# Kernel tuning notes

Measured on AMD Instinct MI355X. Metric: run time of the kernel, lower is better.

Reference implementation:

```python
import jax, jax.numpy as jnp
import numpy as np

B = 32; NPG = 290; N = B * NPG; EPG = 2320; E = B * EPG
LP = 900; IN_FEATS = 75; D = 128; HD = 256; K = 3; HK = HD * K; HOUT = 2


def setup_inputs() -> dict:
    key = jax.random.key(0)
    ks = jax.random.split(key, 20)
    s = 0.05
    rng = np.random.default_rng(0)
    off = np.arange(B)[:, None] * NPG  # keep edges inside each graph block
    edge_src = jnp.asarray((rng.integers(0, NPG, (B, EPG)) + off).reshape(-1), dtype=jnp.int32)
    edge_dst = jnp.asarray((rng.integers(0, NPG, (B, EPG)) + off).reshape(-1), dtype=jnp.int32)
    node_h = jax.random.normal(ks[0], (N, IN_FEATS), jnp.float32)
    v_p = jax.random.randint(ks[1], (B, LP), 0, 26, jnp.int32)
    W_init = (jax.random.normal(ks[2], (IN_FEATS, D)) * s).at[:, -1].set(0.0)  # padding unit zeroed
    gcn_W = jax.random.normal(ks[3], (3, 3, D, D)) * s
    gcn_b = jnp.zeros((3, 3, D))
    gcn_Wres = jax.random.normal(ks[4], (3, 3, D, D)) * s
    gcn_bres = jnp.zeros((3, 3, D))
    emb = (jax.random.normal(ks[5], (26, D)) * s).at[0].set(0.0)  # padding_idx=0
    conv1_w = jax.random.normal(ks[6], (D, D, 3)) * s
    conv2_w = jax.random.normal(ks[7], (D, D, 6)) * s
    conv3_w = jax.random.normal(ks[8], (D, D, 9)) * s
    conv_b = jnp.zeros((3, D))
    cnn_bn_g = jnp.ones((3, D)); cnn_bn_b = jnp.zeros((3, D))
    Wv = jax.random.normal(ks[9], (D, HK)) * s; bv = jnp.zeros((HK,))
    Wq = jax.random.normal(ks[10], (D, HK)) * s; bq = jnp.zeros((HK,))
    h_mat = jax.random.normal(ks[11], (HOUT, HK)) * s
    h_bias = jnp.zeros((HOUT,))
    ban_bn_g = jnp.ones((HD,)); ban_bn_b = jnp.zeros((HD,))
    m_w1 = jax.random.normal(ks[12], (HD, 512)) * s; m_b1 = jnp.zeros((512,))
    m_w2 = jax.random.normal(ks[13], (512, 512)) * s; m_b2 = jnp.zeros((512,))
    m_w3 = jax.random.normal(ks[14], (512, 128)) * s; m_b3 = jnp.zeros((128,))
    m_w4 = jax.random.normal(ks[15], (128, 1)) * s; m_b4 = jnp.zeros((1,))
    mbn_g1 = jnp.ones((512,)); mbn_b1 = jnp.zeros((512,))
    mbn_g2 = jnp.ones((512,)); mbn_b2 = jnp.zeros((512,))
    mbn_g3 = jnp.ones((128,)); mbn_b3 = jnp.zeros((128,))
    return dict(node_h=node_h, edge_src=edge_src, edge_dst=edge_dst, v_p=v_p,
                W_init=W_init, gcn_W=gcn_W, gcn_b=gcn_b, gcn_Wres=gcn_Wres, gcn_bres=gcn_bres,
                emb=emb, conv1_w=conv1_w, conv2_w=conv2_w, conv3_w=conv3_w, conv_b=conv_b,
                cnn_bn_g=cnn_bn_g, cnn_bn_b=cnn_bn_b, Wv=Wv, bv=bv, Wq=Wq, bq=bq,
                h_mat=h_mat, h_bias=h_bias, ban_bn_g=ban_bn_g, ban_bn_b=ban_bn_b,
                m_w1=m_w1, m_b1=m_b1, m_w2=m_w2, m_b2=m_b2, m_w3=m_w3, m_b3=m_b3,
                m_w4=m_w4, m_b4=m_b4, mbn_g1=mbn_g1, mbn_b1=mbn_b1, mbn_g2=mbn_g2,
                mbn_b2=mbn_b2, mbn_g3=mbn_g3, mbn_b3=mbn_b3)


def _bn_feat(x, g, b):  # BatchNorm1d on [B, C], training-mode batch stats
    m = jnp.mean(x, 0); v = jnp.var(x, 0)
    return (x - m) * jax.lax.rsqrt(v + 1e-5) * g + b


def _bn_chan(x, g, b):  # BatchNorm1d on [B, C, L]
    m = jnp.mean(x, (0, 2), keepdims=True); v = jnp.var(x, (0, 2), keepdims=True)
    return (x - m) * jax.lax.rsqrt(v + 1e-5) * g[None, :, None] + b[None, :, None]


def _forward(node_h, W_init, gcn_W, gcn_b, gcn_Wres, gcn_bres, emb, conv1_w, conv2_w,
             conv3_w, conv_b, cnn_bn_g, cnn_bn_b, Wv, bv, Wq, bq, h_mat, h_bias,
             ban_bn_g, ban_bn_b, m_w1, m_b1, m_w2, m_b2, m_w3, m_b3, m_w4, m_b4,
             mbn_g1, mbn_b1, mbn_g2, mbn_b2, mbn_g3, mbn_b3, edge_src, edge_dst, v_p):
    relu = jax.nn.relu

    def gcn(h, W, b, Wr, br):  # 3 dgllife GCN layers: sum-aggregate + relu + residual
        for l in range(3):
            agg = jax.ops.segment_sum(h[edge_src], edge_dst, num_segments=N)
            h = relu(agg @ W[l] + b[l]) + relu(h @ Wr[l] + br[l])
        return h

    h0 = node_h @ W_init  # shared init_transform (no bias)
    v_d_o = gcn(h0, gcn_W[0], gcn_b[0], gcn_Wres[0], gcn_bres[0]).reshape(B, NPG, D)
    pos1 = gcn(h0, gcn_W[1], gcn_b[1], gcn_Wres[1], gcn_bres[1]).reshape(B, NPG, D)
    pos2 = gcn(h0, gcn_W[2], gcn_b[2], gcn_Wres[2], gcn_bres[2]).reshape(B, NPG, D)

    x = emb[v_p].transpose(0, 2, 1)  # [B, D, LP]
    dn = ('NCH', 'OIH', 'NCH')
    for w, cb, g, bb in ((conv1_w, conv_b[0], cnn_bn_g[0], cnn_bn_b[0]),
                         (conv2_w, conv_b[1], cnn_bn_g[1], cnn_bn_b[1]),
                         (conv3_w, conv_b[2], cnn_bn_g[2], cnn_bn_b[2])):
        x = jax.lax.conv_general_dilated(x, w, (1,), 'VALID', dimension_numbers=dn) + cb[None, :, None]
        x = _bn_chan(relu(x), g, bb)
    v_p_o = x.transpose(0, 2, 1)  # [B, 885, D]

    q_ = relu(v_p_o @ Wq + bq)  # BAN q_net (shared across views)

    def ban(vd):  # BANLayer forward (eval-mode dropout)
        v_ = relu(vd @ Wv + bv)  # [B, Nv, HK]
        att = jnp.einsum('hk,bvk,bqk->bhvq', h_mat, v_, q_) + h_bias[None, :, None, None]
        f = jnp.einsum('bvk,bhvq,bqk->bk', v_, att, q_)  # summed over h_out heads
        f = f.reshape(-1, HD, K).sum(-1)  # AvgPool1d(k) * k == sum over k groups
        return _bn_feat(f, ban_bn_g, ban_bn_b)

    def mlp(f):
        f = _bn_feat(relu(f @ m_w1 + m_b1), mbn_g1, mbn_b1)
        f = _bn_feat(relu(f @ m_w2 + m_b2), mbn_g2, mbn_b2)
        f = _bn_feat(relu(f @ m_w3 + m_b3), mbn_g3, mbn_b3)
        return f @ m_w4 + m_b4

    f_o = ban(v_d_o)  # Transformer_lar treated as identity -> beta blend is a no-op
    score_o = mlp(f_o)
    s1 = mlp(ban(pos1))
    s2 = mlp(ban(pos2))

    def norm(z):
        return z / jnp.maximum(jnp.linalg.norm(z, axis=1, keepdims=True), 1e-12)

    km = norm(s1) @ norm(s2).T  # cosine_similarity_kernel
    loss = -jnp.mean(jnp.diagonal(jax.nn.log_softmax(km, axis=1)))  # CE vs arange labels
    return jnp.concatenate([score_o, s1, s2, loss * jnp.ones((B, 1), score_o.dtype)], axis=1)


def reference(node_h, edge_src, edge_dst, v_p, W_init, gcn_W, gcn_b, gcn_Wres, gcn_bres,
              emb, conv1_w, conv2_w, conv3_w, conv_b, cnn_bn_g, cnn_bn_b, Wv, bv, Wq, bq,
              h_mat, h_bias, ban_bn_g, ban_bn_b, m_w1, m_b1, m_w2, m_b2, m_w3, m_b3,
              m_w4, m_b4, mbn_g1, mbn_b1, mbn_g2, mbn_b2, mbn_g3, mbn_b3):
    return _forward(node_h, W_init, gcn_W, gcn_b, gcn_Wres, gcn_bres, emb, conv1_w,
                    conv2_w, conv3_w, conv_b, cnn_bn_g, cnn_bn_b, Wv, bv, Wq, bq,
                    h_mat, h_bias, ban_bn_g, ban_bn_b, m_w1, m_b1, m_w2, m_b2, m_w3,
                    m_b3, m_w4, m_b4, mbn_g1, mbn_b1, mbn_g2, mbn_b2, mbn_g3, mbn_b3,
                    edge_src, edge_dst, v_p)
```

## Files before the change

### kernel.cpp

```cpp
#include <hip/hip_runtime.h>
#include <hip/hip_bf16.h>

#define Bc 32
#define NPGc 290
#define Nn 9280
#define Ec 74240
#define LPc 900
#define INFc 75
#define Dd 128
#define HKc 768
#define LQ 885
#define S1 904
#define S2 896
#define S3 888
#define NT 78
#define TSZ 4096

typedef __attribute__((ext_vector_type(8))) short bf16x8;
typedef __attribute__((ext_vector_type(16))) float f32x16;

static __device__ __forceinline__ unsigned short f2bf(float v){
  unsigned int u = __float_as_uint(v);
  unsigned int r = u + 0x7FFFu + ((u >> 16) & 1u);
  return (unsigned short)(r >> 16);
// ... 46 lines not shown
}

__global__ void k_aggm(unsigned short* __restrict__ aggH, unsigned short* __restrict__ aggL,
                       const float* __restrict__ inb, size_t istride,
                       const float* __restrict__ Adj){
  int g = blockIdx.z, b = blockIdx.y;
  int i0 = blockIdx.x*64;
  const float* h = inb + (size_t)g*istride + (size_t)b*NPGc*Dd;
  const float* Ab = Adj + (size_t)b*NPGc*NPGc;
  __shared__ unsigned short Bh[128*24], Bl[128*24];
  int tid = threadIdx.x;
  int w = tid>>6, l = tid&63, lr = l&31, lg = l>>5;
  int mh = w>>1, nh = w&1;
  int kr = tid>>4, jq = tid&15;
  f32x16 acc0={}, acc1={};
  for (int c=0;c<19;c++){
    int k0 = c*16;
    {
      int ci = k0 + kr;
      if (ci < NPGc){
        const float* hr_ = h + (size_t)ci*Dd + jq*8;
        #pragma unroll
        for (int m=0;m<8;m++){
          float v = hr_[m];
          unsigned short hi16 = f2bf(v);
          Bh[(jq*8+m)*24 + kr] = hi16;
          Bl[(jq*8+m)*24 + kr] = f2bf(v - bf2f(hi16));
        }
      } else {
        #pragma unroll
        for (int m=0;m<8;m++){ Bh[(jq*8+m)*24+kr]=0; Bl[(jq*8+m)*24+kr]=0; }
      }
    }
    __syncthreads();
    int row = i0 + mh*32 + lr;
    bf16x8 aA = {0,0,0,0,0,0,0,0};
    if (row < NPGc && k0+15 < NPGc){
      const float* ar_ = Ab + (size_t)row*NPGc + k0 + lg*8;
      #pragma unroll
      for (int m=0;m<8;m++) aA[m] = (short)f2bf(ar_[m]);
    } else if (row < NPGc){
      #pragma unroll
      for (int m=0;m<8;m++){
        int k = k0 + lg*8 + m;
        aA[m] = (short)((k < NPGc) ? f2bf(Ab[(size_t)row*NPGc + k]) : 0);
      }
    }
    bf16x8 b0H = *(const bf16x8*)&Bh[(nh*64+lr)*24 + lg*8];
    bf16x8 b0L = *(const bf16x8*)&Bl[(nh*64+lr)*24 + lg*8];
    bf16x8 b1H = *(const bf16x8*)&Bh[(nh*64+32+lr)*24 + lg*8];
    bf16x8 b1L = *(const bf16x8*)&Bl[(nh*64+32+lr)*24 + lg*8];
    acc0 = __builtin_amdgcn_mfma_f32_32x32x16_bf16(aA, b0H, acc0, 0, 0, 0);
    acc0 = __builtin_amdgcn_mfma_f32_32x32x16_bf16(aA, b0L, acc0, 0, 0, 0);
    acc1 = __builtin_amdgcn_mfma_f32_32x32x16_bf16(aA, b1H, acc1, 0, 0, 0);
    acc1 = __builtin_amdgcn_mfma_f32_32x32x16_bf16(aA, b1L, acc1, 0, 0, 0);
    __syncthreads();
  }
  size_t gb = ((size_t)g*Bc + b)*NPGc;
  int j0 = nh*64 + lr;
  #pragma unroll
  for (int reg=0; reg<16; reg++){
    int rowl = (reg&3) + 8*(reg>>2) + 4*lg;
    int i = i0 + mh*32 + rowl;
    if (i < NPGc){
      size_t base = (gb + i)*Dd;
      float v0 = acc0[reg];
      unsigned short h0_ = f2bf(v0);
      aggH[base + j0] = h0_;
      aggL[base + j0] = f2bf(v0 - bf2f(h0_));
      float v1 = acc1[reg];
      unsigned short h1_ = f2bf(v1);
      aggH[base + j0 + 32] = h1_;
      aggL[base + j0 + 32] = f2bf(v1 - bf2f(h1_));
    }
  }
}

__global__ void k_gcnlin(float* __restrict__ outb, size_t ostride,
                         const unsigned short* __restrict__ aggH, const unsigned short* __restrict__ aggL,
                         const float* __restrict__ inb, size_t istride,
                         const unsigned short* __restrict__ WTs, const unsigned short* __restrict__ WrTs,
                         const float* __restrict__ ball, const float* __restrict__ brall, int lno){
  int g = blockIdx.y;
  int m0 = blockIdx.x*64;
  int gl = g*3 + lno;
  const size_t NW = (size_t)9*8*Dd*16;
  int tid = threadIdx.x;
  int w=tid>>6, l=tid&63, lr=l&31, lg=l>>5;
  int mh=w>>1, nh=w&1;
  const float* hin = inb + (size_t)g*istride;
  const unsigned short* agH = aggH + (size_t)g*Nn*Dd;
  const unsigned short* agL = aggL + (size_t)g*Nn*Dd;
  f32x16 aw0={},aw1={},ar0={},ar1={};
  int row = m0 + mh*32 + lr;
  for (int c=0;c<8;c++){
    int k0 = c*16;
    bf16x8 gH = *(const bf16x8*)&agH[(size_t)row*Dd + k0 + lg*8];
    bf16x8 gL = *(const bf16x8*)&agL[(size_t)row*Dd + k0 + lg*8];
    bf16x8 hH, hL;
    {
      const float* hp = hin + (size_t)row*Dd + k0 + lg*8;
      #pragma unroll
      for (int m=0;m<8;m++){
        float v = hp[m];
        unsigned short x = f2bf(v);
        hH[m] = (short)x;
        hL[m] = (short)f2bf(v - bf2f(x));
      }
    }
    size_t wb0 = ((((size_t)gl*8 + c)*Dd) + nh*64 + lr)*16 + (size_t)lg*8;
    size_t wb1 = wb0 + 32*16;
    bf16x8 w0H = *(const bf16x8*)&WTs[wb0];
    bf16x8 w0L = *(const bf16x8*)&WTs[NW + wb0];
    bf16x8 w1H = *(const bf16x8*)&WTs[wb1];
    bf16x8 w1L = *(const bf16x8*)&WTs[NW + wb1];
    bf16x8 r0H = *(const bf16x8*)&WrTs[wb0];
    bf16x8 r0L = *(const bf16x8*)&WrTs[NW + wb0];
    bf16x8 r1H = *(const bf16x8*)&WrTs[wb1];
    bf16x8 r1L = *(const bf16x8*)&WrTs[NW + wb1];
    aw0 = __builtin_amdgcn_mfma_f32_32x32x16_bf16(gH, w0H, aw0, 0,0,0);
    aw0 = __builtin_amdgcn_mfma_f32_32x32x16_bf16(gH, w0L, aw0, 0,0,0);
    aw0 = __builtin_amdgcn_mfma_f32_32x32x16_bf16(gL, w0H, aw0, 0,0,0);
    aw1 = __builtin_amdgcn_mfma_f32_32x32x16_bf16(gH, w1H, aw1, 0,0,0);
    aw1 = __builtin_amdgcn_mfma_f32_32x32x16_bf16(gH, w1L, aw1, 0,0,0);
    aw1 = __builtin_amdgcn_mfma_f32_32x32x16_bf16(gL, w1H, aw1, 0,0,0);
    ar0 = __builtin_amdgcn_mfma_f32_32x32x16_bf16(hH, r0H, ar0, 0,0,0);
    ar0 = __builtin_amdgcn_mfma_f32_32x32x16_bf16(hH, r0L, ar0, 0,0,0);
    ar0 = __builtin_amdgcn_mfma_f32_32x32x16_bf16(hL, r0H, ar0, 0,0,0);
    ar1 = __builtin_amdgcn_mfma_f32_32x32x16_bf16(hH, r1H, ar1, 0,0,0);
    ar1 = __builtin_amdgcn_mfma_f32_32x32x16_bf16(hH, r1L, ar1, 0,0,0);
    ar1 = __builtin_amdgcn_mfma_f32_32x32x16_bf16(hL, r1H, ar1, 0,0,0);
  }
  float* out = outb + (size_t)g*ostride;
  int j0 = nh*64 + lr;
  float b0 = ball[gl*Dd + j0], b1 = ball[gl*Dd + j0 + 32];
  float c0 = brall[gl*Dd + j0], c1 = brall[gl*Dd + j0 + 32];
  #pragma unroll
  for (int reg=0; reg<16; reg++){
    int rowl = (reg&3)+8*(reg>>2)+4*lg;
    int i = m0 + mh*32 + rowl;
    out[(size_t)i*Dd + j0]      = fmaxf(aw0[reg]+b0,0.f) + fmaxf(ar0[reg]+c0,0.f);
    out[(size_t)i*Dd + j0 + 32] = fmaxf(aw1[reg]+b1,0.f) + fmaxf(ar1[reg]+c1,0.f);
  }
}

__global__ void k_embed(float* __restrict__ x, const int* __restrict__ vp, const float* __restrict__ emb){
  int t = blockIdx.x*blockDim.x + threadIdx.x;
  int d = blockIdx.y, b = blockIdx.z;
  if (t >= LPc) return;
  int tok = vp[b*LPc + t];
  x[((size_t)b*Dd + d)*LPc + t] = emb[(size_t)tok*Dd + d];
}

__global__ void k_wpack(unsigned short* __restrict__ wp, const float* __restrict__ w, int KW, int C){
  int idx = blockIdx.x*256 + threadIdx.x;
  int tot = C*128*24;
  if (idx >= tot) return;
  int c = idx / (128*24);
  int r = idx - c*128*24;
  int o = r / 24, s = r - o*24;
  float v = 0.f;
  if (s < 16){
    int k = c*16 + s;
    int i = k / KW, kw = k - i*KW;
    v = w[((size_t)o*Dd + i)*KW + kw];
  }
  unsigned short hi = f2bf(v);
  unsigned short lo = f2bf(v - bf2f(hi));
  wp[(size_t)c*3072 + o*24 + s] = hi;
  wp[(size_t)C*3072 + (size_t)c*3072 + o*24 + s] = lo;
}

template<int KW>
__global__ void k_convmfma(float* __restrict__ y, const float* __restrict__ x,
                           const unsigned short* __restrict__ wp,
                           const float* __restrict__ cb, const float* __restrict__ scale,
                           const float* __restrict__ shift,
                           int Lin, int Lout, int XS, int YS, int cbo){
  const int C = (Dd*KW)/16;
  int b = blockIdx.y;
  int t0 = blockIdx.x*64;
  __shared__ unsigned short Ah[128*24], Al[128*24], Bh[64*24], Bl[64*24];
  int tid = threadIdx.x;
  int w = tid >> 6, l = tid & 63;
  int lr = l & 31, lg = l >> 5;
  int kx = tid & 15, tq = tid >> 4;
  f32x16 acc0 = {};
  f32x16 acc1 = {};
  const unsigned short* wlo = wp + (size_t)C*3072;
  for (int c=0; c<C; c++){
    {
      const unsigned int* sh_ = (const unsigned int*)(wp  + (size_t)c*3072);
      const unsigned int* sl_ = (const unsigned int*)(wlo + (size_t)c*3072);
      unsigned int* dh = (unsigned int*)Ah;
      unsigned int* dl = (unsigned int*)Al;
      #pragma unroll
      for (int it=0; it<6; it++){
        int o2 = it*256 + tid;
        dh[o2] = sh_[o2];
        dl[o2] = sl_[o2];
      }
    }
    {
      int k = c*16 + kx;
      int i = k / KW, kw = k - i*KW;
      float sc_ = scale ? scale[i] : 1.f;
      float sh2 = shift ? shift[i] : 0.f;
      const float* xr = x + ((size_t)b*Dd + i)*XS + kw + t0 + tq*4;
      int tb = t0 + tq*4 + kw;
      #pragma unroll
      for (int j2=0; j2<4; j2++){
        float v = (tb + j2 < Lin) ? xr[j2]*sc_ + sh2 : 0.f;
        unsigned short h16 = f2bf(v);
        unsigned short l16 = f2bf(v - bf2f(h16));
        Bh[(tq*4+j2)*24 + kx] = h16;
        Bl[(tq*4+j2)*24 + kx] = l16;
      }
    }
    __syncthreads();
    bf16x8 aH  = *(const bf16x8*)&Ah[(w*32+lr)*24 + lg*8];
    bf16x8 aL  = *(const bf16x8*)&Al[(w*32+lr)*24 + lg*8];
    bf16x8 b0H = *(const bf16x8*)&Bh[lr*24 + lg*8];
    bf16x8 b0L = *(const bf16x8*)&Bl[lr*24 + lg*8];
    bf16x8 b1H = *(const bf16x8*)&Bh[(32+lr)*24 + lg*8];
    bf16x8 b1L = *(const bf16x8*)&Bl[(32+lr)*24 + lg*8];
    acc0 = __builtin_amdgcn_mfma_f32_32x32x16_bf16(aH, b0H, acc0, 0, 0, 0);
    acc1 = __builtin_amdgcn_mfma_f32_32x32x16_bf16(aH, b1H, acc1, 0, 0, 0);
    acc0 = __builtin_amdgcn_mfma_f32_32x32x16_bf16(aH, b0L, acc0, 0, 0, 0);
    acc1 = __builtin_amdgcn_mfma_f32_32x32x16_bf16(aH, b1L, acc1, 0, 0, 0);
    acc0 = __builtin_amdgcn_mfma_f32_32x32x16_bf16(aL, b0H, acc0, 0, 0, 0);
    acc1 = __builtin_amdgcn_mfma_f32_32x32x16_bf16(aL, b1H, acc1, 0, 0, 0);
    __syncthreads();
  }
  int tc = t0 + lr;
  #pragma unroll
  for (int reg=0; reg<16; reg++){
    int row = (reg&3) + 8*(reg>>2) + 4*lg;
    int o = w*32 + row;
    float bias = cb[cbo + o];
    float* yp = y + ((size_t)b*Dd + o)*YS;
    if (tc < Lout)      yp[tc]      = fmaxf(acc0[reg] + bias, 0.f);
    if (tc + 32 < Lout) yp[tc + 32] = fmaxf(acc1[reg] + bias, 0.f);
  }
}

__global__ void k_bnc_stats2(float* __restrict__ scale, float* __restrict__ shift,
                             const float* __restrict__ y, int Lout, int YS,
                             const float* __restrict__ g, const float* __restrict__ bb, int go){
  int c = blockIdx.x;
  float s=0.f, ss=0.f;
  int cnt = Bc*Lout;
  for (int i = threadIdx.x; i < cnt; i += blockDim.x){
    int b = i / Lout, t = i - b*Lout;
    float v = y[((size_t)b*Dd+c)*YS + t];
    s += v; ss += v*v;
  }
  __shared__ float rs[256], rss[256];
  rs[threadIdx.x]=s; rss[threadIdx.x]=ss; __syncthreads();
  for (int st=128; st>0; st>>=1){
    if (threadIdx.x<st){ rs[threadIdx.x]+=rs[threadIdx.x+st]; rss[threadIdx.x]+=rss[threadIdx.x+st]; }
    __syncthreads();
  }
  if (threadIdx.x==0){
    float m = rs[0]/cnt; float v = rss[0]/cnt - m*m; if (v<0.f) v=0.f;
    float r = rsqrtf(v+1e-5f);
    float scl = r*g[go+c];
    scale[c] = scl;
    shift[c] = bb[go+c] - m*scl;
  }
}

__global__ void k_qgemm_tile(float* __restrict__ qc, const float* __restrict__ x,
                             const float* __restrict__ W, const float* __restrict__ bias,
                             const float* __restrict__ scale, const float* __restrict__ shift,
                             int gbase){
  int bl = blockIdx.z, b = gbase + bl;
  int m0 = blockIdx.y*64;
  int n0 = blockIdx.x*64;
  __shared__ float As[16][64], Bs[16][64];
  int tid = threadIdx.x;
  int tx = tid & 15, ty = tid >> 4;
  int ldr = tid >> 4, ldc = (tid & 15)*4;
  float acc[4][4] = {};
  for (int k0 = 0; k0 < Dd; k0 += 16){
    int d = k0 + ldr;
    float sc_ = scale[d], sh_ = shift[d];
    const float* xrow = x + ((size_t)b*Dd + d)*S3 + m0 + ldc;
    int mb = m0 + ldc;
    float4 a4;
    a4.x = (mb+0 < LQ) ? xrow[0]*sc_+sh_ : 0.f;
    a4.y = (mb+1 < LQ) ? xrow[1]*sc_+sh_ : 0.f;
    a4.z = (mb+2 < LQ) ? xrow[2]*sc_+sh_ : 0.f;
    a4.w = (mb+3 < LQ) ? xrow[3]*sc_+sh_ : 0.f;
    *(float4*)&As[ldr][ldc] = a4;
    *(float4*)&Bs[ldr][ldc] = *(const float4*)(W + (size_t)d*HKc + n0 + ldc);
    __syncthreads();
    #pragma unroll
    for (int kk=0; kk<16; kk++){
      float a[4], bb[4];
      *(float4*)a  = *(const float4*)&As[kk][ty*4];
      *(float4*)bb = *(const float4*)&Bs[kk][tx*4];
      #pragma unroll
      for (int i=0;i<4;i++)
        #pragma unroll
        for (int j=0;j<4;j++) acc[i][j] += a[i]*bb[j];
    }
    __syncthreads();
  }
  #pragma unroll
  for (int i=0;i<4;i++){
    int m = m0 + ty*4 + i;
    if (m >= LQ) continue;
    int n = n0 + tx*4;
    float4 b4 = *(const float4*)(bias + n);
    float4 o;
    o.x = fmaxf(acc[i][0] + b4.x, 0.f);
    o.y = fmaxf(acc[i][1] + b4.y, 0.f);
    o.z = fmaxf(acc[i][2] + b4.z, 0.f);
    o.w = fmaxf(acc[i][3] + b4.w, 0.f);
    *(float4*)(qc + ((size_t)bl*LQ + m)*HKc + n) = o;
  }
}

__global__ void k_colsum_q(float* __restrict__ S, const float* __restrict__ X, int gbase){
  int j = blockIdx.x*256 + threadIdx.x;
  int bl = blockIdx.y;
  if (j >= HKc) return;
  const float* p = X + (size_t)bl*LQ*HKc + j;
  float s=0.f;
  for (int t=0;t<LQ;t++) s += p[(size_t)t*HKc];
  S[(gbase+bl)*HKc + j] = s;
}

__global__ void k_gram_sym(float* __restrict__ Gp, const float* __restrict__ X, int gbase){
  int bl = blockIdx.y, bg = gbase + bl;
  int tl0 = blockIdx.x;
  int tl = tl0; int ti = 0;
  while (tl >= 12-ti){ tl -= 12-ti; ti++; }
  int tj = ti + tl;
  int r0 = ti*64, c0 = tj*64;
  const float* Xb = X + (size_t)bl*LQ*HKc;
  float* Gb = Gp + ((size_t)bg*NT + tl0)*TSZ;
  __shared__ float As[16][64], Bs[16][64];
  int tid = threadIdx.x;
  int tx = tid & 15, ty = tid >> 4;
  int ldr = tid >> 4, ldc = (tid & 15)*4;
  float acc[4][4] = {};
  for (int t0=0; t0<LQ; t0+=16){
    float4 av = make_float4(0.f,0.f,0.f,0.f), bv4 = make_float4(0.f,0.f,0.f,0.f);
    if (t0+ldr < LQ){
      const float* row = Xb + (size_t)(t0+ldr)*HKc;
      av  = *(const float4*)(row + r0 + ldc);
      bv4 = *(const float4*)(row + c0 + ldc);
    }
    *(float4*)&As[ldr][ldc] = av;
    *(float4*)&Bs[ldr][ldc] = bv4;
    __syncthreads();
    #pragma unroll
    for (int tt=0; tt<16; tt++){
      float a[4], bb[4];
      *(float4*)a  = *(const float4*)&As[tt][ty*4];
      *(float4*)bb = *(const float4*)&Bs[tt][tx*4];
      #pragma unroll
      for (int i=0;i<4;i++)
        #pragma unroll
        for (int j=0;j<4;j++) acc[i][j] += a[i]*bb[j];
    }
    __syncthreads();
  }
  for (int i=0;i<4;i++){
    int rl = ty*4 + i;
    *(float4*)(Gb + rl*64 + tx*4) =
      make_float4(acc[i][0],acc[i][1],acc[i][2],acc[i][3]);
  }
}

__global__ void k_vgemm8(float* __restrict__ v, const float* __restrict__ vd,
                         const float* __restrict__ W, const float* __restrict__ bias){
  int j = blockIdx.x*256 + threadIdx.x;
  int r0 = blockIdx.y*8;
  __shared__ float xr[8][Dd];
  for (int idx=threadIdx.x; idx<8*Dd; idx+=256){
    int r = idx>>7, k = idx&127;
    xr[r][k] = vd[(size_t)(r0 + r)*Dd + k];
  }
  __syncthreads();
  float acc[8];
  float bj = bias[j];
  #pragma unroll
  for (int r=0;r<8;r++) acc[r]=bj;
  for (int k=0;k<Dd;k++){
    float wk = W[(size_t)k*HKc+j];
    #pragma unroll
    for (int r=0;r<8;r++) acc[r] += xr[r][k]*wk;
  }
  #pragma unroll
  for (int r=0;r<8;r++)
    v[(size_t)(r0+r)*HKc + j] = fmaxf(acc[r],0.f);
}

__global__ void k_colsum_v(float* __restrict__ S, const float* __restrict__ X){
  int j = blockIdx.x*blockDim.x + threadIdx.x;
  int bl = blockIdx.y;
  if (j >= HKc) return;
  const float* p = X + (size_t)bl*NPGc*HKc + j;
  float s=0.f;
  for (int t=0;t<NPGc;t++) s += p[(size_t)t*HKc];
  S[bl*HKc + j] = s;
}

__global__ void k_gramf_sym(float* __restrict__ f, const float* __restrict__ V,
                            const float* __restrict__ Gp, const float* __restrict__ hm){
  int bg = blockIdx.z;
  int tl0 = blockIdx.x;
  int tl = tl0; int ti = 0;
  while (tl >= 12-ti){ tl -= 12-ti; ti++; }
  int tj = ti + tl;
  int r0 = ti*64, c0 = tj*64;
  int offdiag = (ti != tj);
  const float* Vb = V + (size_t)bg*NPGc*HKc;
  __shared__ float As[16][64], Bs[16][64];
  __shared__ float wc[64], wr[64];
  int tid = threadIdx.x;
  int tx = tid & 15, ty = tid >> 4;
  int ldr = tid >> 4, ldc = (tid & 15)*4;
  if (tid < 64) wc[tid] = hm[c0+tid] + hm[HKc + c0 + tid];
  else if (tid < 128) wr[tid-64] = hm[r0+tid-64] + hm[HKc + r0 + tid-64];
  float acc[4][4] = {};
  for (int t0=0; t0<NPGc; t0+=16){
    float4 av = make_float4(0.f,0.f,0.f,0.f), bv4 = make_float4(0.f,0.f,0.f,0.f);
    if (t0+ldr < NPGc){
      const float* row = Vb + (size_t)(t0+ldr)*HKc;
      av  = *(const float4*)(row + r0 + ldc);
      bv4 = *(const float4*)(row + c0 + ldc);
    }
    *(float4*)&As[ldr][ldc] = av;
    *(float4*)&Bs[ldr][ldc] = bv4;
    __syncthreads();
    #pragma unroll
    for (int tt=0; tt<16; tt++){
      float a[4], bb[4];
      *(float4*)a  = *(const float4*)&As[tt][ty*4];
      *(float4*)bb = *(const float4*)&Bs[tt][tx*4];
      #pragma unroll
      for (int i=0;i<4;i++)
        #pragma unroll
        for (int j=0;j<4;j++) acc[i][j] += a[i]*bb[j];
    }
    __syncthreads();
  }
  const float* gqb = Gp + ((size_t)bg*NT + tl0)*TSZ;
  float w0 = wc[tx*4+0], w1 = wc[tx*4+1], w2 = wc[tx*4+2], w3 = wc[tx*4+3];
  float colp[4] = {0.f,0.f,0.f,0.f};
  #pragma unroll
  for (int i=0;i<4;i++){
    int rl = ty*4 + i;
    int r = r0 + rl;
    const float4 g4 = *(const float4*)(gqb + rl*64 + tx*4);
    float s = acc[i][0]*w0*g4.x + acc[i][1]*w1*g4.y
            + acc[i][2]*w2*g4.z + acc[i][3]*w3*g4.w;
    s += __shfl_xor(s, 1); s += __shfl_xor(s, 2);
    s += __shfl_xor(s, 4); s += __shfl_xor(s, 8);
    if (tx==0) atomicAdd(&f[bg*HKc + r], s);
    if (offdiag){
      float wri = wr[rl];
      colp[0] += acc[i][0]*wri*g4.x;
      colp[1] += acc[i][1]*wri*g4.y;
      colp[2] += acc[i][2]*wri*g4.z;
      colp[3] += acc[i][3]*wri*g4.w;
    }
  }
  if (offdiag){
    #pragma unroll
    for (int j=0;j<4;j++){
      colp[j] += __shfl_xor(colp[j], 16);
      colp[j] += __shfl_xor(colp[j], 32);
    }
    if ((tid & 48) == 0){
      #pragma unroll
      for (int j=0;j<4;j++)
        atomicAdd(&f[bg*HKc + c0 + tx*4 + j], colp[j]);
    }
  }
}

__global__ void k_pool3(float* __restrict__ fp, const float* __restrict__ f3,
                        const float* __restrict__ Sv3, const float* __restrict__ Sq,
                        const float* __restrict__ hb){
  int idx = blockIdx.x*256 + threadIdx.x;
  if (idx >= 3*Bc*256) return;
  int v = idx >> 13;
  int rem = idx & 8191;
  int b = rem >> 8, c = rem & 255;
  const float* f = f3 + (size_t)v*Bc*HKc;
  const float* Sv = Sv3 + (size_t)v*Bc*HKc;
  float hbs = hb[0] + hb[1];
  float s = 0.f;
  #pragma unroll
  for (int r=0;r<3;r++){
    int k = c*3 + r;
    s += f[b*HKc + k] + hbs*Sv[b*HKc + k]*Sq[b*HKc + k];
  }
  fp[idx] = s;
}

__global__ void k_bnfeat3(float* __restrict__ y, const float* __restrict__ x, const float* __restrict__ g,
                          const float* __restrict__ bb, int C){
  int c = blockIdx.x; int v = blockIdx.y; int b = threadIdx.x;
  __shared__ float buf[32];
  __shared__ float mv[2];
  int row = v*32 + b;
  float val = x[(size_t)row*C + c];
  buf[b] = val;
  __syncthreads();
  if (b == 0){
    float s = 0.f;
    for (int i=0;i<32;i++) s += buf[i];
    float m = s/32.f;
    float vs = 0.f;
    for (int i=0;i<32;i++){ float d = buf[i]-m; vs += d*d; }
    mv[0] = m; mv[1] = vs/32.f;
  }
  __syncthreads();
  y[(size_t)row*C + c] = (val - mv[0])*rsqrtf(mv[1]+1e-5f)*g[c] + bb[c];
}

__global__ void k_mlp(float* __restrict__ out, const float* __restrict__ in, const float* __restrict__ W,
                      const float* __restrict__ bias, int K, int Nc, int doRelu){
  int b = blockIdx.y;
  int j = blockIdx.x*blockDim.x + threadIdx.x;
  __shared__ float xr[512];
  for (int k=threadIdx.x; k<K; k+=blockDim.x) xr[k] = in[(size_t)b*K+k];
  __syncthreads();
  if (j >= Nc) return;
  float s = bias[j];
  for (int k=0;k<K;k++) s += xr[k]*W[(size_t)k*Nc + j];
  if (doRelu) s = fmaxf(s, 0.f);
  out[(size_t)b*Nc + j] = s;
}

__global__ void k_score96(float* __restrict__ sc, const float* __restrict__ h, const float* __restrict__ w,
                          const float* __restrict__ bb){
  int b = threadIdx.x; if (b>=96) return;
  float s = bb[0];
  for (int k=0;k<Dd;k++) s += h[(size_t)b*Dd+k]*w[k];
  sc[b] = s;
}

__global__ void k_out(float* __restrict__ out, const float* __restrict__ scores){
  int t = threadIdx.x;
  __shared__ float loss_s;
  if (t == 0){
    float sn1[32], sn2[32];
    for (int i=0;i<32;i++){
      float a = scores[32+i]; sn1[i] = a / fmaxf(fabsf(a), 1e-12f);
      float c = scores[64+i]; sn2[i] = c / fmaxf(fabsf(c), 1e-12f);
    }
    float acc = 0.f;
    for (int i=0;i<32;i++){
      float mx = -1e30f;
      for (int j=0;j<32;j++) mx = fmaxf(mx, sn1[i]*sn2[j]);
      float se = 0.f;
      for (int j=0;j<32;j++) se += expf(sn1[i]*sn2[j]-mx);
      acc += sn1[i]*sn2[i] - (mx + logf(se));
    }
    loss_s = -acc/32.f;
  }
  __syncthreads();
  out[t*4+0] = scores[t];
  out[t*4+1] = scores[32+t];
  out[t*4+2] = scores[64+t];
  out[t*4+3] = loss_s;
}

extern "C" void kernel_launch(void* const* d_in, const int* in_sizes, int n_in,
                              void* d_out, int out_size, void* d_ws, size_t ws_size,
                              hipStream_t stream){
  static const int exp_sizes[38] = {
    Nn*INFc, Ec, Ec, Bc*LPc, INFc*Dd,
    9*Dd*Dd, 9*Dd, 9*Dd*Dd, 9*Dd,
    26*Dd, Dd*Dd*3, Dd*Dd*6, Dd*Dd*9, 3*Dd, 3*Dd, 3*Dd,
    Dd*HKc, HKc, Dd*HKc, HKc, 2*HKc, 2, 256, 256,
    256*512, 512, 512*512, 512, 512*128, 128, 128, 1,
    512, 512, 512, 512, 128, 128 };
  if (n_in != 38){ k_sentinel<<<1,128,0,stream>>>((float*)d_out, 2000.f + n_in); return; }
  for (int i=0;i<38;i++){
    if (in_sizes[i] != exp_sizes[i]){
      k_sentinel<<<1,128,0,stream>>>((float*)d_out, 1000.f + i); return;
    }
  }

  const float* node_h=(const float*)d_in[0];
  const int*  esrc  =(const int*)d_in[1];
  const int*  edst  =(const int*)d_in[2];
  const int*  vp    =(const int*)d_in[3];
  const float* W_init=(const float*)d_in[4];
  const float* gcn_W =(const float*)d_in[5];
  const float* gcn_b =(const float*)d_in[6];
  const float* gcn_Wr=(const float*)d_in[7];
  const float* gcn_br=(const float*)d_in[8];
  const float* emb   =(const float*)d_in[9];
  const float* c1w=(const float*)d_in[10];
  const float* c2w=(const float*)d_in[11];
  const float* c3w=(const float*)d_in[12];
  const float* cbv=(const float*)d_in[13];
  const float* bng=(const float*)d_in[14];
  const float* bnb=(const float*)d_in[15];
  const float* Wv =(const float*)d_in[16];
  const float* bvv=(const float*)d_in[17];
  const float* Wq =(const float*)d_in[18];
  const float* bq =(const float*)d_in[19];
  const float* hmat =(const float*)d_in[20];
  const float* hbias=(const float*)d_in[21];
  const float* bang =(const float*)d_in[22];
  const float* banb =(const float*)d_in[23];
  const float* mw1=(const float*)d_in[24]; const float* mb1=(const float*)d_in[25];
  const float* mw2=(const float*)d_in[26]; const float* mb2=(const float*)d_in[27];
  const float* mw3=(const float*)d_in[28]; const float* mb3=(const float*)d_in[29];
  const float* mw4=(const float*)d_in[30]; const float* mb4=(const float*)d_in[31];
  const float* g1=(const float*)d_in[32]; const float* bb1=(const float*)d_in[33];
  const float* g2=(const float*)d_in[34]; const float* bb2=(const float*)d_in[35];
  const float* g3=(const float*)d_in[36]; const float* bb3=(const float*)d_in[37];

  float* ws = (float*)d_ws;
  size_t off = 0;
  auto alloc = [&](size_t n){ float* p = ws + off; off += n; return p; };

  const size_t NDsz = (size_t)Nn*Dd;
  const size_t CNNBP = (size_t)Bc*Dd*S1;
  const size_t ADJ  = (size_t)Bc*NPGc*NPGc;
  const size_t QB8  = (size_t)8*LQ*HKc;
  const size_t VB   = (size_t)Bc*NPGc*HKc;
  const size_t AGGF = (size_t)3*Nn*Dd;
  size_t ARENA = 7*NDsz + ADJ + AGGF;
  if (ARENA < 4*NDsz + VB) ARENA = 4*NDsz + VB;
  if (ARENA < CNNBP + QB8) ARENA = CNNBP + QB8;
  if (ARENA < 2*CNNBP) ARENA = 2*CNNBP;

  float* Sq   = alloc((size_t)Bc*HKc);
  float* Sv3  = alloc((size_t)3*Bc*HKc);
  float* fbuf3= alloc((size_t)3*Bc*HKc);
  float* fpool3=alloc((size_t)3*Bc*256);
  float* hh1  = alloc((size_t)96*512);
  float* hh2  = alloc((size_t)96*512);
  float* hh3  = alloc((size_t)96*128);
  float* sc   = alloc(96);
  float* scl1 = alloc(128); float* shf1 = alloc(128);
  float* scl2 = alloc(128); float* shf2 = alloc(128);
  float* scl3 = alloc(128); float* shf3 = alloc(128);
  unsigned short* wp1 = (unsigned short*)alloc((size_t)24*3072);
  unsigned short* wp2 = (unsigned short*)alloc((size_t)48*3072);
  unsigned short* wp3 = (unsigned short*)alloc((size_t)72*3072);
  unsigned short* WTs  = (unsigned short*)alloc(147456);
  unsigned short* WrTs = (unsigned short*)alloc(147456);
  float* Gqp = alloc((size_t)Bc*NT*TSZ);
  float* arena = alloc(ARENA);

  float* cnnA = arena;
  float* cnnB = arena + CNNBP;
  float* qbuf = arena + CNNBP;
  float* h0b  = arena;
  float* Bb   = arena + NDsz;
  float* Cb   = arena + 4*NDsz;
  float* Adj  = arena + 7*NDsz;
  unsigned short* aggH = (unsigned short*)(arena + 7*NDsz + ADJ);
  unsigned short* aggL = aggH + (size_t)3*Nn*Dd;
  float* vbuf = arena + 4*NDsz;


  k_wpack<<<(24*128*24+255)/256,256,0,stream>>>(wp1, c1w, 3, 24);
  k_wpack<<<(48*128*24+255)/256,256,0,stream>>>(wp2, c2w, 6, 48);
  k_wpack<<<(72*128*24+255)/256,256,0,stream>>>(wp3, c3w, 9, 72);
  k_wsplit<<<(9*Dd*Dd+255)/256,256,0,stream>>>(WTs, WrTs, gcn_W, gcn_Wr);

  k_embed<<<dim3((LPc+127)/128, Dd, Bc),128,0,stream>>>(cnnB, vp, emb);
  k_convmfma<3><<<dim3(15,Bc),256,0,stream>>>(cnnA, cnnB, wp1, cbv, nullptr, nullptr, 900, 898, 900, S1, 0);
  k_bnc_stats2<<<Dd,256,0,stream>>>(scl1, shf1, cnnA, 898, S1, bng, bnb, 0);
  k_convmfma<6><<<dim3(14,Bc),256,0,stream>>>(cnnB, cnnA, wp2, cbv, scl1, shf1, 898, 893, S1, S2, 128);
  k_bnc_stats2<<<Dd,256,0,stream>>>(scl2, shf2, cnnB, 893, S2, bng, bnb, 128);
  k_convmfma<9><<<dim3(14,Bc),256,0,stream>>>(cnnA, cnnB, wp3, cbv, scl2, shf2, 893, 885, S2, S3, 256);
  k_bnc_stats2<<<Dd,256,0,stream>>>(scl3, shf3, cnnA, 885, S3, bng, bnb, 256);

  for (int gb = 0; gb < Bc; gb += 8){
    k_qgemm_tile<<<dim3(12,(LQ+63)/64,8),256,0,stream>>>(qbuf, cnnA, Wq, bq, scl3, shf3, gb);
    k_colsum_q<<<dim3(3,8),256,0,stream>>>(Sq, qbuf, gb);
    k_gram_sym<<<dim3(NT,8),256,0,stream>>>(Gqp, qbuf, gb);
  }

  hipMemsetAsync(Adj, 0, ADJ*sizeof(float), stream);
  k_build_adj<<<(Ec+255)/256,256,0,stream>>>(Adj, esrc, edst);

  hipMemsetAsync(fbuf3, 0, (size_t)3*Bc*HKc*sizeof(float), stream);

  k_h0<<<Nn,Dd,0,stream>>>(h0b, node_h, W_init);
  k_aggm<<<dim3(5,Bc,3),256,0,stream>>>(aggH, aggL, h0b, 0, Adj);
  k_gcnlin<<<dim3(145,3),256,0,stream>>>(Bb, NDsz, aggH, aggL, h0b, 0, WTs, WrTs, gcn_b, gcn_br, 0);
  k_aggm<<<dim3(5,Bc,3),256,0,stream>>>(aggH, aggL, Bb, NDsz, Adj);
  k_gcnlin<<<dim3(145,3),256,0,stream>>>(Cb, NDsz, aggH, aggL, Bb, NDsz, WTs, WrTs, gcn_b, gcn_br, 1);
  k_aggm<<<dim3(5,Bc,3),256,0,stream>>>(aggH, aggL, Cb, NDsz, Adj);
  k_gcnlin<<<dim3(145,3),256,0,stream>>>(Bb, NDsz, aggH, aggL, Cb, NDsz, WTs, WrTs, gcn_b, gcn_br, 2);

  for (int g=0; g<3; g++){
    k_vgemm8<<<dim3(3,(Bc*NPGc)/8),256,0,stream>>>(vbuf, Bb + (size_t)g*NDsz, Wv, bvv);
    k_colsum_v<<<dim3(3,Bc),256,0,stream>>>(Sv3 + (size_t)g*Bc*HKc, vbuf);
    k_gramf_sym<<<dim3(NT,1,Bc),256,0,stream>>>(fbuf3 + (size_t)g*Bc*HKc, vbuf, Gqp, hmat);
  }

  k_pool3<<<(3*Bc*256+255)/256,256,0,stream>>>(fpool3, fbuf3, Sv3, Sq, hbias);
  k_bnfeat3<<<dim3(256,3),32,0,stream>>>(fpool3, fpool3, bang, banb, 256);
  k_mlp<<<dim3(2,96),256,0,stream>>>(hh1, fpool3, mw1, mb1, 256, 512, 1);
  k_bnfeat3<<<dim3(512,3),32,0,stream>>>(hh1, hh1, g1, bb1, 512);
  k_mlp<<<dim3(2,96),256,0,stream>>>(hh2, hh1, mw2, mb2, 512, 512, 1);
  k_bnfeat3<<<dim3(512,3),32,0,stream>>>(hh2, hh2, g2, bb2, 512);
  k_mlp<<<dim3(1,96),256,0,stream>>>(hh3, hh2, mw3, mb3, 512, 128, 1);
  k_bnfeat3<<<dim3(128,3),32,0,stream>>>(hh3, hh3, g3, bb3, 128);
  k_score96<<<1,96,0,stream>>>(sc, hh3, mw4, mb4);
  k_out<<<1,32,0,stream>>>((float*)d_out, sc);
}
```

Baseline: 1.856 ms.

## Move Q gram to split-bf16 MFMA, fold BN into conv weights, double-buffer conv

The FP32 FMA Gram kernel over the Q projections is replaced with an MFMA kernel. It uses a hi/lo bf16 split that the qgemm epilogue now writes directly. The conv layers fold the previous batch-norm scale and shift into packed weights and a precomputed bias, so per-element scaling and bounds checks leave the inner loop. Conv A-operands are now read straight from global memory, and the B tile is double-buffered in LDS with a register prefetch. The split-bf16 products drop the lo*lo term, which slightly changes numerics, and the folded weights must be repacked after each stats pass.

```diff
diff --git a/kernel.cpp b/kernel.cpp
--- a/kernel.cpp
+++ b/kernel.cpp
@@ -222,84 +222,98 @@
   x[((size_t)b*Dd + d)*LPc + t] = emb[(size_t)tok*Dd + d];
 }
 
-__global__ void k_wpack(unsigned short* __restrict__ wp, const float* __restrict__ w, int KW, int C){
+__global__ void k_wpack16(unsigned short* __restrict__ wp, const float* __restrict__ w,
+                          const float* __restrict__ scale, int KW, int C){
   int idx = blockIdx.x*256 + threadIdx.x;
-  int tot = C*128*24;
+  int tot = C*2048;
   if (idx >= tot) return;
-  int c = idx / (128*24);
-  int r = idx - c*128*24;
-  int o = r / 24, s = r - o*24;
-  float v = 0.f;
-  if (s < 16){
-    int k = c*16 + s;
-    int i = k / KW, kw = k - i*KW;
-    v = w[((size_t)o*Dd + i)*KW + kw];
-  }
+  int c = idx >> 11;
+  int r = idx & 2047;
+  int o = r >> 4, s = r & 15;
+  int k = c*16 + s;
+  int i = k / KW, kw = k - i*KW;
+  float v = w[((size_t)o*Dd + i)*KW + kw];
+  if (scale) v *= scale[i];
   unsigned short hi = f2bf(v);
-  unsigned short lo = f2bf(v - bf2f(hi));
-  wp[(size_t)c*3072 + o*24 + s] = hi;
-  wp[(size_t)C*3072 + (size_t)c*3072 + o*24 + s] = lo;
+  wp[idx] = hi;
+  wp[(size_t)tot + idx] = f2bf(v - bf2f(hi));
+}
+
+__global__ void k_bfold(float* __restrict__ bout, const float* __restrict__ w,
+                        const float* __restrict__ shf, const float* __restrict__ cb,
+                        int go, int KW){
+  int o = blockIdx.x, i = threadIdx.x;
+  float p = 0.f;
+  if (shf){
+    const float* wr = w + ((size_t)o*Dd + i)*KW;
+    float s = 0.f;
+    for (int kw=0; kw<KW; kw++) s += wr[kw];
+    p = s * shf[i];
+  }
+  __shared__ float red[128];
+  red[i] = p; __syncthreads();
+  for (int st=64; st>0; st>>=1){
+    if (i<st) red[i] += red[i+st];
+    __syncthreads();
+  }
+  if (i==0) bout[o] = cb[go+o] + red[0];
 }
 
 template<int KW>
-__global__ void k_convmfma(float* __restrict__ y, const float* __restrict__ x,
-                           const unsigned short* __restrict__ wp,
-                           const float* __restrict__ cb, const float* __restrict__ scale,
-                           const float* __restrict__ shift,
-                           int Lin, int Lout, int XS, int YS, int cbo){
+__global__ void k_convmfma2(float* __restrict__ y, const float* __restrict__ x,
+                            const unsigned short* __restrict__ wp,
+                            const float* __restrict__ biasF,
+                            int Lout, int XS, int YS){
   const int C = (Dd*KW)/16;
   int b = blockIdx.y;
   int t0 = blockIdx.x*64;
-  __shared__ unsigned short Ah[128*24], Al[128*24], Bh[64*24], Bl[64*24];
+  __shared__ unsigned short Bh[2][64*24], Bl[2][64*24];
   int tid = threadIdx.x;
-  int w = tid >> 6, l = tid & 63;
-  int lr = l & 31, lg = l >> 5;
-  int kx = tid & 15, tq = tid >> 4;
-  f32x16 acc0 = {};
-  f32x16 acc1 = {};
-  const unsigned short* wlo = wp + (size_t)C*3072;
-  for (int c=0; c<C; c++){
-    {
-      const unsigned int* sh_ = (const unsigned int*)(wp  + (size_t)c*3072);
-      const unsigned int* sl_ = (const unsigned int*)(wlo + (size_t)c*3072);
-      unsigned int* dh = (unsigned int*)Ah;
-      unsigned int* dl = (unsigned int*)Al;
-      #pragma unroll
-      for (int it=0; it<6; it++){
-        int o2 = it*256 + tid;
-        dh[o2] = sh_[o2];
-        dl[o2] = sl_[o2];
-      }
-    }
-    {
-      int k = c*16 + kx;
-      int i = k / KW, kw = k - i*KW;
-      float sc_ = scale ? scale[i] : 1.f;
-      float sh2 = shift ? shift[i] : 0.f;
-      const float* xr = x + ((size_t)b*Dd + i)*XS + kw + t0 + tq*4;
-      int tb = t0 + tq*4 + kw;
-      #pragma unroll
-      for (int j2=0; j2<4; j2++){
-        float v = (tb + j2 < Lin) ? xr[j2]*sc_ + sh2 : 0.f;
-        unsigned short h16 = f2bf(v);
-        unsigned short l16 = f2bf(v - bf2f(h16));
-        Bh[(tq*4+j2)*24 + kx] = h16;
-        Bl[(tq*4+j2)*24 + kx] = l16;
-      }
-    }
-    __syncthreads();
-    bf16x8 aH  = *(const bf16x8*)&Ah[(w*32+lr)*24 + lg*8];
-    bf16x8 aL  = *(const bf16x8*)&Al[(w*32+lr)*24 + lg*8];
-    bf16x8 b0H = *(const bf16x8*)&Bh[lr*24 + lg*8];
-    bf16x8 b0L = *(const bf16x8*)&Bl[lr*24 + lg*8];
-    bf16x8 b1H = *(const bf16x8*)&Bh[(32+lr)*24 + lg*8];
-    bf16x8 b1L = *(const bf16x8*)&Bl[(32+lr)*24 + lg*8];
-    acc0 = __builtin_amdgcn_mfma_f32_32x32x16_bf16(aH, b0H, acc0, 0, 0, 0);
-    acc1 = __builtin_amdgcn_mfma_f32_32x32x16_bf16(aH, b1H, acc1, 0, 0, 0);
-    acc0 = __builtin_amdgcn_mfma_f32_32x32x16_bf16(aH, b0L, acc0, 0, 0, 0);
-    acc1 = __builtin_amdgcn_mfma_f32_32x32x16_bf16(aH, b1L, acc1, 0, 0, 0);
-    acc0 = __builtin_amdgcn_mfma_f32_32x32x16_bf16(aL, b0H, acc0, 0, 0, 0);
-    acc1 = __builtin_amdgcn_mfma_f32_32x32x16_bf16(aL, b1H, acc1, 0, 0, 0);
+  int w = tid>>6, l = tid&63, lr = l&31, lg = l>>5;
+  int kx = tid&15, tq = tid>>4;
+  const unsigned short* wpL = wp + (size_t)C*2048;
+  const float* xb = x + (size_t)b*Dd*XS;
+  f32x16 acc0={}, acc1={};
+  {
+    int i = kx/KW, kw = kx - i*KW;
+    const float* xr = xb + (size_t)i*XS + t0 + kw + tq*4;
+    #pragma unroll
+    for (int j=0;j<4;j++){
+      float v = xr[j];
+      unsigned short h = f2bf(v);
+      Bh[0][(tq*4+j)*24+kx] = h;
+      Bl[0][(tq*4+j)*24+kx] = f2bf(v - bf2f(h));
+    }
+  }
+  __syncthreads();
+  for (int c=0;c<C;c++){
+    int cur = c&1, nxt = cur^1;
+    bf16x8 aH = *(const bf16x8*)(wp  + ((size_t)c*128 + w*32+lr)*16 + lg*8);
+    bf16x8 aL = *(const bf16x8*)(wpL + ((size_t)c*128 + w*32+lr)*16 + lg*8);
+    float pv0=0.f,pv1=0.f,pv2=0.f,pv3=0.f;
+    if (c+1<C){
+      int k1 = (c+1)*16 + kx;
+      int i = k1/KW, kw = k1 - i*KW;
+      const float* xr = xb + (size_t)i*XS + t0 + kw + tq*4;
+      pv0 = xr[0]; pv1 = xr[1]; pv2 = xr[2]; pv3 = xr[3];
+    }
+    bf16x8 b0H = *(const bf16x8*)&Bh[cur][lr*24 + lg*8];
+    bf16x8 b0L = *(const bf16x8*)&Bl[cur][lr*24 + lg*8];
+    bf16x8 b1H = *(const bf16x8*)&Bh[cur][(32+lr)*24 + lg*8];
+    bf16x8 b1L = *(const bf16x8*)&Bl[cur][(32+lr)*24 + lg*8];
+    acc0 = __builtin_amdgcn_mfma_f32_32x32x16_bf16(aH, b0H, acc0, 0,0,0);
+    acc1 = __builtin_amdgcn_mfma_f32_32x32x16_bf16(aH, b1H, acc1, 0,0,0);
+    acc0 = __builtin_amdgcn_mfma_f32_32x32x16_bf16(aH, b0L, acc0, 0,0,0);
+    acc1 = __builtin_amdgcn_mfma_f32_32x32x16_bf16(aH, b1L, acc1, 0,0,0);
+    acc0 = __builtin_amdgcn_mfma_f32_32x32x16_bf16(aL, b0H, acc0, 0,0,0);
+    acc1 = __builtin_amdgcn_mfma_f32_32x32x16_bf16(aL, b1H, acc1, 0,0,0);
+    if (c+1<C){
+      unsigned short h;
+      h = f2bf(pv0); Bh[nxt][(tq*4+0)*24+kx]=h; Bl[nxt][(tq*4+0)*24+kx]=f2bf(pv0-bf2f(h));
+      h = f2bf(pv1); Bh[nxt][(tq*4+1)*24+kx]=h; Bl[nxt][(tq*4+1)*24+kx]=f2bf(pv1-bf2f(h));
+      h = f2bf(pv2); Bh[nxt][(tq*4+2)*24+kx]=h; Bl[nxt][(tq*4+2)*24+kx]=f2bf(pv2-bf2f(h));
+      h = f2bf(pv3); Bh[nxt][(tq*4+3)*24+kx]=h; Bl[nxt][(tq*4+3)*24+kx]=f2bf(pv3-bf2f(h));
+    }
     __syncthreads();
   }
   int tc = t0 + lr;
@@ -307,7 +321,7 @@
   for (int reg=0; reg<16; reg++){
     int row = (reg&3) + 8*(reg>>2) + 4*lg;
     int o = w*32 + row;
-    float bias = cb[cbo + o];
+    float bias = biasF[o];
     float* yp = y + ((size_t)b*Dd + o)*YS;
     if (tc < Lout)      yp[tc]      = fmaxf(acc0[reg] + bias, 0.f);
     if (tc + 32 < Lout) yp[tc + 32] = fmaxf(acc1[reg] + bias, 0.f);
@@ -340,7 +354,8 @@
   }
 }
 
-__global__ void k_qgemm_tile(float* __restrict__ qc, const float* __restrict__ x,
+__global__ void k_qgemm_tile(unsigned short* __restrict__ qH, unsigned short* __restrict__ qL,
+                             const float* __restrict__ x,
                              const float* __restrict__ W, const float* __restrict__ bias,
                              const float* __restrict__ scale, const float* __restrict__ shift,
                              int gbase){
@@ -383,65 +398,104 @@
     if (m >= LQ) continue;
     int n = n0 + tx*4;
     float4 b4 = *(const float4*)(bias + n);
-    float4 o;
-    o.x = fmaxf(acc[i][0] + b4.x, 0.f);
-    o.y = fmaxf(acc[i][1] + b4.y, 0.f);
-    o.z = fmaxf(acc[i][2] + b4.z, 0.f);
-    o.w = fmaxf(acc[i][3] + b4.w, 0.f);
-    *(float4*)(qc + ((size_t)bl*LQ + m)*HKc + n) = o;
-  }
-}
-
-__global__ void k_colsum_q(float* __restrict__ S, const float* __restrict__ X, int gbase){
+    float o0 = fmaxf(acc[i][0] + b4.x, 0.f);
+    float o1 = fmaxf(acc[i][1] + b4.y, 0.f);
+    float o2 = fmaxf(acc[i][2] + b4.z, 0.f);
+    float o3 = fmaxf(acc[i][3] + b4.w, 0.f);
+    ushort4 sh, sl;
+    sh.x = f2bf(o0); sl.x = f2bf(o0 - bf2f(sh.x));
+    sh.y = f2bf(o1); sl.y = f2bf(o1 - bf2f(sh.y));
+    sh.z = f2bf(o2); sl.z = f2bf(o2 - bf2f(sh.z));
+    sh.w = f2bf(o3); sl.w = f2bf(o3 - bf2f(sh.w));
+    size_t base = ((size_t)bl*LQ + m)*HKc + n;
+    *(ushort4*)(qH + base) = sh;
+    *(ushort4*)(qL + base) = sl;
+  }
+}
+
+__global__ void k_colsum_q(float* __restrict__ S, const unsigned short* __restrict__ qH,
+                           const unsigned short* __restrict__ qL, int gbase){
   int j = blockIdx.x*256 + threadIdx.x;
   int bl = blockIdx.y;
   if (j >= HKc) return;
-  const float* p = X + (size_t)bl*LQ*HKc + j;
+  const unsigned short* ph = qH + (size_t)bl*LQ*HKc + j;
+  const unsigned short* pl = qL + (size_t)bl*LQ*HKc + j;
   float s=0.f;
-  for (int t=0;t<LQ;t++) s += p[(size_t)t*HKc];
+  for (int t=0;t<LQ;t++) s += bf2f(ph[(size_t)t*HKc]) + bf2f(pl[(size_t)t*HKc]);
   S[(gbase+bl)*HKc + j] = s;
 }
 
-__global__ void k_gram_sym(float* __restrict__ Gp, const float* __restrict__ X, int gbase){
+__global__ void k_gram_mfma(float* __restrict__ Gp, const unsigned short* __restrict__ qH,
+                            const unsigned short* __restrict__ qL, int gbase){
   int bl = blockIdx.y, bg = gbase + bl;
   int tl0 = blockIdx.x;
   int tl = tl0; int ti = 0;
   while (tl >= 12-ti){ tl -= 12-ti; ti++; }
   int tj = ti + tl;
   int r0 = ti*64, c0 = tj*64;
-  const float* Xb = X + (size_t)bl*LQ*HKc;
+  const unsigned short* qHb = qH + (size_t)bl*LQ*HKc;
+  const unsigned short* qLb = qL + (size_t)bl*LQ*HKc;
   float* Gb = Gp + ((size_t)bg*NT + tl0)*TSZ;
-  __shared__ float As[16][64], Bs[16][64];
+  __shared__ unsigned short Ah[2][64*24], Al[2][64*24], Bh[2][64*24], Bl[2][64*24];
   int tid = threadIdx.x;
-  int tx = tid & 15, ty = tid >> 4;
-  int ldr = tid >> 4, ldc = (tid & 15)*4;
-  float acc[4][4] = {};
-  for (int t0=0; t0<LQ; t0+=16){
-    float4 av = make_float4(0.f,0.f,0.f,0.f), bv4 = make_float4(0.f,0.f,0.f,0.f);
-    if (t0+ldr < LQ){
-      const float* row = Xb + (size_t)(t0+ldr)*HKc;
-      av  = *(const float4*)(row + r0 + ldc);
-      bv4 = *(const float4*)(row + c0 + ldc);
-    }
-    *(float4*)&As[ldr][ldc] = av;
-    *(float4*)&Bs[ldr][ldc] = bv4;
-    __syncthreads();
-    #pragma unroll
-    for (int tt=0; tt<16; tt++){
-      float a[4], bb[4];
-      *(float4*)a  = *(const float4*)&As[tt][ty*4];
-      *(float4*)bb = *(const float4*)&Bs[tt][tx*4];
-      #pragma unroll
-      for (int i=0;i<4;i++)
-        #pragma unroll
-        for (int j=0;j<4;j++) acc[i][j] += a[i]*bb[j];
-    }
-    __syncthreads();
-  }
-  for (int i=0;i<4;i++){
-    int rl = ty*4 + i;
-    *(float4*)(Gb + rl*64 + tx*4) =
-      make_float4(acc[i][0],acc[i][1],acc[i][2],acc[i][3]);
+  int w = tid>>6, l = tid&63, lr = l&31, lg = l>>5;
+  int mi = w>>1, ni = w&1;
+  int kr = tid>>4, cg = tid&15;
+  const int C = (LQ+15)/16;
+  f32x16 acc = {};
+  {
+    ushort4 z = {0,0,0,0};
+    ushort4 ah=z, al=z, bh=z, bl_=z;
+    if (kr < LQ){
+      const unsigned short* rh = qHb + (size_t)kr*HKc;
+      const unsigned short* rl = qLb + (size_t)kr*HKc;
+      ah  = *(const ushort4*)(rh + r0 + cg*4);
+      al  = *(const ushort4*)(rl + r0 + cg*4);
+      bh  = *(const ushort4*)(rh + c0 + cg*4);
+      bl_ = *(const ushort4*)(rl + c0 + cg*4);
+    }
+    int b0 = (cg*4)*24 + kr;
+    Ah[0][b0]=ah.x; Ah[0][b0+24]=ah.y; Ah[0][b0+48]=ah.z; Ah[0][b0+72]=ah.w;
+    Al[0][b0]=al.x; Al[0][b0+24]=al.y; Al[0][b0+48]=al.z; Al[0][b0+72]=al.w;
+    Bh[0][b0]=bh.x; Bh[0][b0+24]=bh.y; Bh[0][b0+48]=bh.z; Bh[0][b0+72]=bh.w;
+    Bl[0][b0]=bl_.x; Bl[0][b0+24]=bl_.y; Bl[0][b0+48]=bl_.z; Bl[0][b0+72]=bl_.w;
+  }
+  __syncthreads();
+  for (int c=0;c<C;c++){
+    int cur=c&1, nxt=cur^1;
+    ushort4 z = {0,0,0,0};
+    ushort4 pah=z, pal=z, pbh=z, pbl=z;
+    if (c+1<C){
+      int t = (c+1)*16 + kr;
+      if (t < LQ){
+        const unsigned short* rh = qHb + (size_t)t*HKc;
+        const unsigned short* rl = qLb + (size_t)t*HKc;
+        pah = *(const ushort4*)(rh + r0 + cg*4);
+        pal = *(const ushort4*)(rl + r0 + cg*4);
+        pbh = *(const ushort4*)(rh + c0 + cg*4);
+        pbl = *(const ushort4*)(rl + c0 + cg*4);
+      }
+    }
+    bf16x8 aH = *(const bf16x8*)&Ah[cur][(mi*32+lr)*24 + lg*8];
+    bf16x8 aL = *(const bf16x8*)&Al[cur][(mi*32+lr)*24 + lg*8];
+    bf16x8 bH = *(const bf16x8*)&Bh[cur][(ni*32+lr)*24 + lg*8];
+    bf16x8 bL = *(const bf16x8*)&Bl[cur][(ni*32+lr)*24 + lg*8];
+    acc = __builtin_amdgcn_mfma_f32_32x32x16_bf16(aH, bH, acc, 0,0,0);
+    acc = __builtin_amdgcn_mfma_f32_32x32x16_bf16(aH, bL, acc, 0,0,0);
+    acc = __builtin_amdgcn_mfma_f32_32x32x16_bf16(aL, bH, acc, 0,0,0);
+    if (c+1<C){
+      int b0 = (cg*4)*24 + kr;
+      Ah[nxt][b0]=pah.x; Ah[nxt][b0+24]=pah.y; Ah[nxt][b0+48]=pah.z; Ah[nxt][b0+72]=pah.w;
+      Al[nxt][b0]=pal.x; Al[nxt][b0+24]=pal.y; Al[nxt][b0+48]=pal.z; Al[nxt][b0+72]=pal.w;
+      Bh[nxt][b0]=pbh.x; Bh[nxt][b0+24]=pbh.y; Bh[nxt][b0+48]=pbh.z; Bh[nxt][b0+72]=pbh.w;
+      Bl[nxt][b0]=pbl.x; Bl[nxt][b0+24]=pbl.y; Bl[nxt][b0+48]=pbl.z; Bl[nxt][b0+72]=pbl.w;
+    }
+    __syncthreads();
+  }
+  #pragma unroll
+  for (int reg=0; reg<16; reg++){
+    int row = (reg&3) + 8*(reg>>2) + 4*lg;
+    Gb[(size_t)(mi*32+row)*64 + ni*32 + lr] = acc[reg];
   }
 }
 
@@ -718,9 +772,10 @@
   float* scl1 = alloc(128); float* shf1 = alloc(128);
   float* scl2 = alloc(128); float* shf2 = alloc(128);
   float* scl3 = alloc(128); float* shf3 = alloc(128);
-  unsigned short* wp1 = (unsigned short*)alloc((size_t)24*3072);
-  unsigned short* wp2 = (unsigned short*)alloc((size_t)48*3072);
-  unsigned short* wp3 = (unsigned short*)alloc((size_t)72*3072);
+  float* b1f  = alloc(128); float* b2f  = alloc(128); float* b3f = alloc(128);
+  unsigned short* wp1 = (unsigned short*)alloc((size_t)384*128);
+  unsigned short* wp2 = (unsigned short*)alloc((size_t)768*128);
+  unsigned short* wp3 = (unsigned short*)alloc((size_t)1152*128);
   unsigned short* WTs  = (unsigned short*)alloc(147456);
   unsigned short* WrTs = (unsigned short*)alloc(147456);
   float* Gqp = alloc((size_t)Bc*NT*TSZ);
@@ -729,6 +784,8 @@
   float* cnnA = arena;
   float* cnnB = arena + CNNBP;
   float* qbuf = arena + CNNBP;
+  unsigned short* qH = (unsigned short*)qbuf;
+  unsigned short* qL = qH + (size_t)8*LQ*HKc;
   float* h0b  = arena;
   float* Bb   = arena + NDsz;
   float* Cb   = arena + 4*NDsz;
@@ -737,24 +794,26 @@
   unsigned short* aggL = aggH + (size_t)3*Nn*Dd;
   float* vbuf = arena + 4*NDsz;
 
-
-  k_wpack<<<(24*128*24+255)/256,256,0,stream>>>(wp1, c1w, 3, 24);
-  k_wpack<<<(48*128*24+255)/256,256,0,stream>>>(wp2, c2w, 6, 48);
-  k_wpack<<<(72*128*24+255)/256,256,0,stream>>>(wp3, c3w, 9, 72);
+  k_wpack16<<<(24*2048+255)/256,256,0,stream>>>(wp1, c1w, nullptr, 3, 24);
+  k_bfold<<<128,128,0,stream>>>(b1f, c1w, nullptr, cbv, 0, 3);
   k_wsplit<<<(9*Dd*Dd+255)/256,256,0,stream>>>(WTs, WrTs, gcn_W, gcn_Wr);
 
   k_embed<<<dim3((LPc+127)/128, Dd, Bc),128,0,stream>>>(cnnB, vp, emb);
-  k_convmfma<3><<<dim3(15,Bc),256,0,stream>>>(cnnA, cnnB, wp1, cbv, nullptr, nullptr, 900, 898, 900, S1, 0);
+  k_convmfma2<3><<<dim3(15,Bc),256,0,stream>>>(cnnA, cnnB, wp1, b1f, 898, 900, S1);
   k_bnc_stats2<<<Dd,256,0,stream>>>(scl1, shf1, cnnA, 898, S1, bng, bnb, 0);
-  k_convmfma<6><<<dim3(14,Bc),256,0,stream>>>(cnnB, cnnA, wp2, cbv, scl1, shf1, 898, 893, S1, S2, 128);
+  k_wpack16<<<(48*2048+255)/256,256,0,stream>>>(wp2, c2w, scl1, 6, 48);
+  k_bfold<<<128,128,0,stream>>>(b2f, c2w, shf1, cbv, 128, 6);
+  k_convmfma2<6><<<dim3(14,Bc),256,0,stream>>>(cnnB, cnnA, wp2, b2f, 893, S1, S2);
   k_bnc_stats2<<<Dd,256,0,stream>>>(scl2, shf2, cnnB, 893, S2, bng, bnb, 128);
-  k_convmfma<9><<<dim3(14,Bc),256,0,stream>>>(cnnA, cnnB, wp3, cbv, scl2, shf2, 893, 885, S2, S3, 256);
+  k_wpack16<<<(72*2048+255)/256,256,0,stream>>>(wp3, c3w, scl2, 9, 72);
+  k_bfold<<<128,128,0,stream>>>(b3f, c3w, shf2, cbv, 256, 9);
+  k_convmfma2<9><<<dim3(14,Bc),256,0,stream>>>(cnnA, cnnB, wp3, b3f, 885, S2, S3);
   k_bnc_stats2<<<Dd,256,0,stream>>>(scl3, shf3, cnnA, 885, S3, bng, bnb, 256);
 
   for (int gb = 0; gb < Bc; gb += 8){
-    k_qgemm_tile<<<dim3(12,(LQ+63)/64,8),256,0,stream>>>(qbuf, cnnA, Wq, bq, scl3, shf3, gb);
-    k_colsum_q<<<dim3(3,8),256,0,stream>>>(Sq, qbuf, gb);
-    k_gram_sym<<<dim3(NT,8),256,0,stream>>>(Gqp, qbuf, gb);
+    k_qgemm_tile<<<dim3(12,(LQ+63)/64,8),256,0,stream>>>(qH, qL, cnnA, Wq, bq, scl3, shf3, gb);
+    k_colsum_q<<<dim3(3,8),256,0,stream>>>(Sq, qH, qL, gb);
+    k_gram_mfma<<<dim3(NT,8),256,0,stream>>>(Gqp, qH, qL, gb);
   }
 
   hipMemsetAsync(Adj, 0, ADJ*sizeof(float), stream);
```

Result: slower. 2.017 ms (+8.7%).
